# Kernel optimization log

Measured on AMD Instinct MI355X. Metric: run time of the kernel, lower is better.

The kernel has to match this reference:

```python
import jax, jax.numpy as jnp
import numpy as np

POSITIVE_EPS = 1e-6  # cfg.positive


def _unnormal_gaussian(loc, H, W):
    # loc: [B, N, 4] = (cx, cy, sx, sy) in normalized [0,1] coords.
    # Returns unnormalized gaussians [B, N, H, W].
    ys = (jnp.arange(H, dtype=loc.dtype) + 0.5) / H  # [H]
    xs = (jnp.arange(W, dtype=loc.dtype) + 0.5) / W  # [W]
    cx = loc[..., 0][..., None, None]
    cy = loc[..., 1][..., None, None]
    sx = loc[..., 2][..., None, None]
    sy = loc[..., 3][..., None, None]
    dx2 = ((xs[None, :] - cx) / sx) ** 2          # [B,N,H,W] via broadcast
    dy2 = ((ys[:, None] - cy) / sy) ** 2
    return jnp.exp(-0.5 * (dx2 + dy2))


def setup_inputs() -> dict:
    key = jax.random.key(0)
    k1, k2, k3, k4, k5 = jax.random.split(key, 5)
    B, N, K, H, W = 8, 200, 32, 138, 138
    Himg, Wimg = 550, 550
    original = jax.random.uniform(k1, (B, 3, Himg, Wimg), dtype=jnp.float32)
    loc = jax.random.uniform(k2, (B, N, 4), dtype=jnp.float32)
    conf = jax.random.uniform(k3, (B, N), dtype=jnp.float32)
    mask = jax.random.normal(k4, (B, N, K), dtype=jnp.float32)
    proto = jax.random.normal(k5, (B, H, W, K), dtype=jnp.float32)
    return {"original": original, "loc": loc, "conf": conf, "mask": mask, "proto": proto}


def reference(original, loc, conf, mask, proto):
    original = original.astype(jnp.float32)
    B, C, Himg, Wimg = original.shape
    H, W = proto.shape[1], proto.shape[2]

    # gaussian.unnormalGaussian over all priors -> [B, N, H, W]
    unnormal = _unnormal_gaussian(loc, H, W)

    # gaussian.lincomb: proto [B,H,W,K] x masks [B,N,K] -> [B,N,H,W], then sigmoid
    assembled = jax.nn.sigmoid(jnp.einsum('bhwk,bnk->bnhw', proto, mask))

    attention = assembled * unnormal                       # [B,N,H,W]
    mask_conf = attention * conf[:, :, None, None]         # einsum abcd,ab->abcd

    denom = jnp.sum(mask_conf, axis=1, keepdims=True) + POSITIVE_EPS
    final_conf = 1.0 - jnp.sum(mask_conf ** 2 / denom, axis=1)  # [B,H,W]

    # F.interpolate bilinear, align_corners=False (half-pixel centers)
    resized_conf = jax.image.resize(final_conf, (B, Himg, Wimg), method='bilinear')

    total_conf = jnp.sum(resized_conf, axis=0)             # [Himg,Wimg]

    weighted_mean = jnp.einsum('bchw,bhw->chw', original, resized_conf)
    squared_diff = (original - weighted_mean[None]) ** 2   # [B,C,Himg,Wimg]
    weighted_diff = squared_diff * resized_conf[:, None]   # einsum abcd,acd->abcd

    weighted_variance = weighted_diff / (total_conf + POSITIVE_EPS)
    return jnp.sum(weighted_variance)
```

## Files before the change

### kernel.cpp

```cpp
#include <hip/hip_runtime.h>
#include <hip/hip_bf16.h>

#define BN 200
#define KK 32
#define NT 13
#define HH 138
#define WW 138
#define HO 550
#define WO 550
#define NPIX (HH*WW)
#define NOUT (HO*WO)
#define EPS 1e-6f
#define LOG2E 1.4426950408889634f

#if __has_builtin(__builtin_amdgcn_rcpf)
#define RCP(x) __builtin_amdgcn_rcpf(x)
#else
#define RCP(x) (1.0f/(x))
#endif
#if __has_builtin(__builtin_amdgcn_exp2f)
#define EXP2(x) __builtin_amdgcn_exp2f(x)
#else
#define EXP2(x) exp2f(x)
#endif

typedef __attribute__((ext_vector_type(8))) short short8v;
typedef __attribute__((ext_vector_type(4))) float f32x4;

static __device__ inline short f2bf(float x) {
    __hip_bfloat16 h = __float2bfloat16(x);
    return *reinterpret_cast<short*>(&h);
}

__global__ __launch_bounds__(256) void k_finalconf(
    const float* __restrict__ loc,
    const float* __restrict__ conf,
    const float* __restrict__ mask,
    const float* __restrict__ proto,
    float* __restrict__ fconf)
{
    const int b   = blockIdx.y;
    const int tid = threadIdx.x;

    __shared__ short sm_bfrag[NT * 64 * 8];
    __shared__ float sm_cx[NT*16], sm_cy[NT*16], sm_isx[NT*16], sm_isy[NT*16], sm_cf[NT*16];

    for (int idx = tid; idx < NT * 64; idx += 256) {
        const int t  = idx >> 6;
        const int l  = idx & 63;
        const int n  = t * 16 + (l & 15);
        const int k0 = (l >> 4) * 8;
        short8v v;
#pragma unroll
        for (int j = 0; j < 8; ++j) v[j] = 0;
        if (n < BN) {
            const float4* src = (const float4*)(mask + ((size_t)b * BN + n) * KK + k0);
            float4 u0 = src[0], u1 = src[1];
            v[0] = f2bf(u0.x); v[1] = f2bf(u0.y); v[2] = f2bf(u0.z); v[3] = f2bf(u0.w);
            v[4] = f2bf(u1.x); v[5] = f2bf(u1.y); v[6] = f2bf(u1.z); v[7] = f2bf(u1.w);
        }
        *(short8v*)&sm_bfrag[idx * 8] = v;
    }
    for (int n = tid; n < NT * 16; n += 256) {
        if (n < BN) {
            float4 l4 = ((const float4*)(loc + (size_t)b * BN * 4))[n];
            sm_cx[n] = l4.x; sm_cy[n] = l4.y;
            sm_isx[n] = RCP(l4.z); sm_isy[n] = RCP(l4.w);
            sm_cf[n] = conf[(size_t)b * BN + n];
        } else {
            sm_cx[n] = 0.5f; sm_cy[n] = 0.5f; sm_isx[n] = 1.0f; sm_isy[n] = 1.0f;
            sm_cf[n] = 0.0f;
        }
    }
    __syncthreads();

    const int wid  = tid >> 6;
    const int lane = tid & 63;
    const int mbase = blockIdx.x * 64 + wid * 16;

    int pa = mbase + (lane & 15);
    if (pa >= NPIX) pa = NPIX - 1;
    const int ka = (lane >> 4) * 8;
    const float4* asrc = (const float4*)(proto + ((size_t)b * NPIX + pa) * KK + ka);
    float4 a0 = asrc[0], a1 = asrc[1];
    short8v afrag;
    afrag[0] = f2bf(a0.x); afrag[1] = f2bf(a0.y); afrag[2] = f2bf(a0.z); afrag[3] = f2bf(a0.w);
    afrag[4] = f2bf(a1.x); afrag[5] = f2bf(a1.y); afrag[6] = f2bf(a1.z); afrag[7] = f2bf(a1.w);

    float xr[4], yr[4];
    int   pr[4];
#pragma unroll
    for (int r = 0; r < 4; ++r) {
        int p = mbase + (lane >> 4) * 4 + r;
        pr[r] = p;
        int pc = p < NPIX ? p : NPIX - 1;
        int h = pc / WW, w = pc - h * WW;
        xr[r] = (w + 0.5f) * (1.0f / WW);
        yr[r] = (h + 0.5f) * (1.0f / HH);
    }

    float sum1[4] = {0.f, 0.f, 0.f, 0.f};
    float sum2[4] = {0.f, 0.f, 0.f, 0.f};

#pragma unroll 2
    for (int t = 0; t < NT; ++t) {
        short8v bfrag = *(const short8v*)&sm_bfrag[(t * 64 + lane) * 8];
        f32x4 c = {0.f, 0.f, 0.f, 0.f};
        c = __builtin_amdgcn_mfma_f32_16x16x32_bf16(afrag, bfrag, c, 0, 0, 0);

        const int n = t * 16 + (lane & 15);
        const float cx = sm_cx[n], cy = sm_cy[n];
        const float isx = sm_isx[n], isy = sm_isy[n], cf = sm_cf[n];
#pragma unroll
        for (int r = 0; r < 4; ++r) {
            const float s  = c[r];
            const float tt = EXP2(-LOG2E * s);
            const float dx = (xr[r] - cx) * isx;
            const float dy = (yr[r] - cy) * isy;
            const float g  = EXP2(-0.5f * LOG2E * fmaf(dx, dx, dy * dy));
            const float mc = g * cf * RCP(1.0f + tt);
            sum1[r] += mc;
            sum2[r] = fmaf(mc, mc, sum2[r]);
        }
    }

#pragma unroll
    for (int m = 1; m < 16; m <<= 1) {
#pragma unroll
        for (int r = 0; r < 4; ++r) {
            sum1[r] += __shfl_xor(sum1[r], m);
            sum2[r] += __shfl_xor(sum2[r], m);
        }
    }

    const int rsel = lane & 15;
#pragma unroll
    for (int r = 0; r < 4; ++r) {
        if (rsel == r && pr[r] < NPIX)
            fconf[(size_t)b * NPIX + pr[r]] = 1.0f - sum2[r] * RCP(sum1[r] + EPS);
    }
}

__global__ __launch_bounds__(256) void k_variance(
    const float* __restrict__ orig,
    const float* __restrict__ fconf,
    float* __restrict__ partial)
{
    const int idx = blockIdx.x * 256 + threadIdx.x;
    float local = 0.0f;

    if (idx < NOUT) {
        const int yo = idx / WO;
        const int xo = idx - yo * WO;
        const float scale = 138.0f / 550.0f;
        float fy = (yo + 0.5f) * scale - 0.5f;
        float fx = (xo + 0.5f) * scale - 0.5f;
        float fy0 = floorf(fy), fx0 = floorf(fx);
        float wy = fy - fy0, wx = fx - fx0;
        int y0 = max(0, min(HH - 1, (int)fy0));
        int y1 = max(0, min(HH - 1, (int)fy0 + 1));
        int x0 = max(0, min(WW - 1, (int)fx0));
        int x1 = max(0, min(WW - 1, (int)fx0 + 1));

        float R[8];
        float T = 0.0f;
#pragma unroll
        for (int b = 0; b < 8; ++b) {
            const float* F = fconf + (size_t)b * NPIX;
            float v00 = F[y0 * WW + x0], v01 = F[y0 * WW + x1];
            float v10 = F[y1 * WW + x0], v11 = F[y1 * WW + x1];
            float v0 = v00 + wx * (v01 - v00);
            float v1 = v10 + wx * (v11 - v10);
            R[b] = v0 + wy * (v1 - v0);
            T += R[b];
        }
        const float invT = RCP(T + EPS);

#pragma unroll
        for (int c = 0; c < 3; ++c) {
            float o[8];
            float M = 0.0f;
#pragma unroll
            for (int b = 0; b < 8; ++b) {
                o[b] = orig[((size_t)b * 3 + c) * NOUT + idx];
                M = fmaf(o[b], R[b], M);
            }
            float s = 0.0f;
#pragma unroll
            for (int b = 0; b < 8; ++b) {
                float d = o[b] - M;
                s = fmaf(d * d, R[b], s);
            }
            local += s * invT;
        }
    }

    __shared__ float red[4];
    const int lane = threadIdx.x & 63;
    const int wid  = threadIdx.x >> 6;
#pragma unroll
    for (int off = 32; off > 0; off >>= 1)
        local += __shfl_down(local, off);
    if (lane == 0) red[wid] = local;
    __syncthreads();
    if (threadIdx.x == 0)
        partial[blockIdx.x] = (red[0] + red[1]) + (red[2] + red[3]);
}

__global__ __launch_bounds__(256) void k_reduce(
    const float* __restrict__ partial, int n, float* __restrict__ out)
{
    float s = 0.0f;
    for (int i = threadIdx.x; i < n; i += 256) s += partial[i];
    __shared__ float red[4];
    const int lane = threadIdx.x & 63;
    const int wid  = threadIdx.x >> 6;
#pragma unroll
    for (int off = 32; off > 0; off >>= 1)
        s += __shfl_down(s, off);
    if (lane == 0) red[wid] = s;
    __syncthreads();
    if (threadIdx.x == 0)
        out[0] = (red[0] + red[1]) + (red[2] + red[3]);
}

extern "C" void kernel_launch(void* const* d_in, const int* in_sizes, int n_in,
                              void* d_out, int out_size, void* d_ws, size_t ws_size,
                              hipStream_t stream) {
    const float* original = (const float*)d_in[0];
    const float* loc      = (const float*)d_in[1];
    const float* conf     = (const float*)d_in[2];
    const float* mask     = (const float*)d_in[3];
    const float* proto    = (const float*)d_in[4];
    float* out = (float*)d_out;

    float* fconf   = (float*)d_ws;
    float* partial = (float*)((char*)d_ws + (size_t)8 * NPIX * sizeof(float));

    dim3 g1((NPIX + 63) / 64, 8);
    k_finalconf<<<g1, 256, 0, stream>>>(loc, conf, mask, proto, fconf);

    const int nb2 = (NOUT + 255) / 256;
    k_variance<<<nb2, 256, 0, stream>>>(original, fconf, partial);

    k_reduce<<<1, 256, 0, stream>>>(partial, nb2, out);
}
```

Measured before the change: 41.73 us.

## Precompute mask fragments and gaussian params in prep kernel, read from global

Adds a small prep kernel that converts the mask coefficients to bf16 MFMA fragments and precomputes the gaussian parameters with the log2e/0.5 scale folded in (scale and offset), writing them to workspace. The finalconf kernel no longer fills shared memory or calls __syncthreads per block and instead reads these precomputed values from global memory (cached) inside a fully unrolled loop. The gaussian exponent now takes two FMAs with no extra multiplies. The cost is an extra kernel launch and global loads in the inner loop instead of LDS reads.

Measured after the change: 39.38 us. 1.06x faster.

```diff
diff --git a/kernel.cpp b/kernel.cpp
--- a/kernel.cpp
+++ b/kernel.cpp
@@ -32,48 +32,60 @@
     return *reinterpret_cast<short*>(&h);
 }
 
-__global__ __launch_bounds__(256) void k_finalconf(
+__global__ __launch_bounds__(256) void k_prep(
     const float* __restrict__ loc,
     const float* __restrict__ conf,
     const float* __restrict__ mask,
+    short8v* __restrict__ bfrag,
+    float4* __restrict__ p4,
+    float*  __restrict__ cf)
+{
+    const int idx = blockIdx.x * 256 + threadIdx.x;
+    if (idx >= 8 * NT * 64) return;
+    const int l  = idx & 63;
+    const int bt = idx >> 6;
+    const int t  = bt % NT;
+    const int b  = bt / NT;
+    const int n  = t * 16 + (l & 15);
+    const int k0 = (l >> 4) * 8;
+
+    short8v v;
+#pragma unroll
+    for (int j = 0; j < 8; ++j) v[j] = 0;
+    if (n < BN) {
+        const float4* src = (const float4*)(mask + ((size_t)b * BN + n) * KK + k0);
+        float4 u0 = src[0], u1 = src[1];
+        v[0] = f2bf(u0.x); v[1] = f2bf(u0.y); v[2] = f2bf(u0.z); v[3] = f2bf(u0.w);
+        v[4] = f2bf(u1.x); v[5] = f2bf(u1.y); v[6] = f2bf(u1.z); v[7] = f2bf(u1.w);
+    }
+    bfrag[idx] = v;
+
+    if (l < 16) {
+        float4 pr = {0.f, 0.f, 0.f, 0.f};
+        float  cv = 0.f;
+        if (n < BN) {
+            const float C = sqrtf(0.5f * LOG2E);
+            float4 l4 = ((const float4*)loc)[(size_t)b * BN + n];
+            float isx = RCP(l4.z) * C;
+            float isy = RCP(l4.w) * C;
+            pr.x = isx; pr.y = isy;
+            pr.z = -l4.x * isx; pr.w = -l4.y * isy;
+            cv = conf[(size_t)b * BN + n];
+        }
+        p4[bt * 16 + (l & 15)] = pr;
+        cf[bt * 16 + (l & 15)] = cv;
+    }
+}
+
+__global__ __launch_bounds__(256) void k_finalconf(
     const float* __restrict__ proto,
+    const short8v* __restrict__ bfrag,
+    const float4* __restrict__ p4,
+    const float*  __restrict__ cf,
     float* __restrict__ fconf)
 {
-    const int b   = blockIdx.y;
-    const int tid = threadIdx.x;
-
-    __shared__ short sm_bfrag[NT * 64 * 8];
-    __shared__ float sm_cx[NT*16], sm_cy[NT*16], sm_isx[NT*16], sm_isy[NT*16], sm_cf[NT*16];
-
-    for (int idx = tid; idx < NT * 64; idx += 256) {
-        const int t  = idx >> 6;
-        const int l  = idx & 63;
-        const int n  = t * 16 + (l & 15);
-        const int k0 = (l >> 4) * 8;
-        short8v v;
-#pragma unroll
-        for (int j = 0; j < 8; ++j) v[j] = 0;
-        if (n < BN) {
-            const float4* src = (const float4*)(mask + ((size_t)b * BN + n) * KK + k0);
-            float4 u0 = src[0], u1 = src[1];
-            v[0] = f2bf(u0.x); v[1] = f2bf(u0.y); v[2] = f2bf(u0.z); v[3] = f2bf(u0.w);
-            v[4] = f2bf(u1.x); v[5] = f2bf(u1.y); v[6] = f2bf(u1.z); v[7] = f2bf(u1.w);
-        }
-        *(short8v*)&sm_bfrag[idx * 8] = v;
-    }
-    for (int n = tid; n < NT * 16; n += 256) {
-        if (n < BN) {
-            float4 l4 = ((const float4*)(loc + (size_t)b * BN * 4))[n];
-            sm_cx[n] = l4.x; sm_cy[n] = l4.y;
-            sm_isx[n] = RCP(l4.z); sm_isy[n] = RCP(l4.w);
-            sm_cf[n] = conf[(size_t)b * BN + n];
-        } else {
-            sm_cx[n] = 0.5f; sm_cy[n] = 0.5f; sm_isx[n] = 1.0f; sm_isy[n] = 1.0f;
-            sm_cf[n] = 0.0f;
-        }
-    }
-    __syncthreads();
-
+    const int b    = blockIdx.y;
+    const int tid  = threadIdx.x;
     const int wid  = tid >> 6;
     const int lane = tid & 63;
     const int mbase = blockIdx.x * 64 + wid * 16;
@@ -99,26 +111,30 @@
         yr[r] = (h + 0.5f) * (1.0f / HH);
     }
 
+    const short8v* BF = bfrag + (size_t)b * NT * 64 + lane;
+    const float4*  PP = p4 + (size_t)b * NT * 16 + (lane & 15);
+    const float*   CV = cf + (size_t)b * NT * 16 + (lane & 15);
+
     float sum1[4] = {0.f, 0.f, 0.f, 0.f};
     float sum2[4] = {0.f, 0.f, 0.f, 0.f};
 
-#pragma unroll 2
+#pragma unroll
     for (int t = 0; t < NT; ++t) {
-        short8v bfrag = *(const short8v*)&sm_bfrag[(t * 64 + lane) * 8];
+        short8v bf = BF[t * 64];
+        float4  pp = PP[t * 16];
+        float   cv = CV[t * 16];
         f32x4 c = {0.f, 0.f, 0.f, 0.f};
-        c = __builtin_amdgcn_mfma_f32_16x16x32_bf16(afrag, bfrag, c, 0, 0, 0);
-
-        const int n = t * 16 + (lane & 15);
-        const float cx = sm_cx[n], cy = sm_cy[n];
-        const float isx = sm_isx[n], isy = sm_isy[n], cf = sm_cf[n];
+        c = __builtin_amdgcn_mfma_f32_16x16x32_bf16(afrag, bf, c, 0, 0, 0);
 #pragma unroll
         for (int r = 0; r < 4; ++r) {
             const float s  = c[r];
             const float tt = EXP2(-LOG2E * s);
-            const float dx = (xr[r] - cx) * isx;
-            const float dy = (yr[r] - cy) * isy;
-            const float g  = EXP2(-0.5f * LOG2E * fmaf(dx, dx, dy * dy));
-            const float mc = g * cf * RCP(1.0f + tt);
+            const float a  = RCP(1.0f + tt);
+            const float dx = fmaf(xr[r], pp.x, pp.z);
+            const float dy = fmaf(yr[r], pp.y, pp.w);
+            const float z  = fmaf(dy, dy, dx * dx);
+            const float g  = EXP2(-z);
+            const float mc = a * g * cv;
             sum1[r] += mc;
             sum2[r] = fmaf(mc, mc, sum2[r]);
         }
@@ -234,13 +250,20 @@
     const float* proto    = (const float*)d_in[4];
     float* out = (float*)d_out;
 
-    float* fconf   = (float*)d_ws;
-    float* partial = (float*)((char*)d_ws + (size_t)8 * NPIX * sizeof(float));
+    const int nb2 = (NOUT + 255) / 256;
+
+    char* ws = (char*)d_ws;
+    float*   fconf   = (float*)ws;                     ws += (size_t)8 * NPIX * sizeof(float);
+    float*   partial = (float*)ws;                     ws += (size_t)nb2 * sizeof(float) + 64;
+    short8v* bfrag   = (short8v*)ws;                   ws += (size_t)8 * NT * 64 * sizeof(short8v);
+    float4*  p4      = (float4*)ws;                    ws += (size_t)8 * NT * 16 * sizeof(float4);
+    float*   cf      = (float*)ws;
+
+    k_prep<<<(8 * NT * 64 + 255) / 256, 256, 0, stream>>>(loc, conf, mask, bfrag, p4, cf);
 
     dim3 g1((NPIX + 63) / 64, 8);
-    k_finalconf<<<g1, 256, 0, stream>>>(loc, conf, mask, proto, fconf);
-
-    const int nb2 = (NOUT + 255) / 256;
+    k_finalconf<<<g1, 256, 0, stream>>>(proto, bfrag, p4, cf, fconf);
+
     k_variance<<<nb2, 256, 0, stream>>>(original, fconf, partial);
 
     k_reduce<<<1, 256, 0, stream>>>(partial, nb2, out);
```
